# Optimization experiments

Hardware: AMD Instinct MI355X
Metric: run time of the kernel (lower is better)

## Reference

```python
import jax, jax.numpy as jnp
import numpy as np

H, D_NOPE, D_ROPE, D_V, L_KV, HID = 16, 128, 64, 128, 512, 2048
D_QK = D_NOPE + D_ROPE
THETA = 10000.0
EPS = 1e-6


def _rope(x, positions):
    # neox-style rotary over last dim (D_ROPE); x: [T, ..., D_ROPE]
    half = D_ROPE // 2
    inv_freq = 1.0 / (THETA ** (jnp.arange(half, dtype=jnp.float32) * 2.0 / D_ROPE))
    ang = positions.astype(jnp.float32)[:, None] * inv_freq[None, :]  # [T, half]
    shape = (x.shape[0],) + (1,) * (x.ndim - 2) + (half,)
    cos, sin = jnp.cos(ang).reshape(shape), jnp.sin(ang).reshape(shape)
    x1, x2 = x[..., :half], x[..., half:]
    return jnp.concatenate([x1 * cos - x2 * sin, x2 * cos + x1 * sin], axis=-1)


def _rmsnorm(x, w):
    var = jnp.mean(x * x, axis=-1, keepdims=True)
    return x * jax.lax.rsqrt(var + EPS) * w


def setup_inputs() -> dict:
    key = jax.random.key(0)
    ks = jax.random.split(key, 6)
    T = 4096
    s = lambda fan_in: 1.0 / np.sqrt(fan_in)
    return {
        "positions": jnp.arange(T, dtype=jnp.int32),
        "hidden_states": jax.random.normal(ks[0], (T, HID), jnp.float32),
        "Wq": jax.random.normal(ks[1], (HID, H * D_QK), jnp.float32) * s(HID),
        "Wkva": jax.random.normal(ks[2], (HID, L_KV + D_ROPE), jnp.float32) * s(HID),
        "kv_a_ln_w": jnp.ones((L_KV,), jnp.float32),
        "Wkvb": jax.random.normal(ks[3], (L_KV, H * (D_NOPE + D_V)), jnp.float32) * s(L_KV),
        "Wo": jax.random.normal(ks[4], (H * D_V, HID), jnp.float32) * s(H * D_V),
    }


def reference(positions, hidden_states, Wq, Wkva, kv_a_ln_w, Wkvb, Wo):
    T = hidden_states.shape[0]
    scaling = 1.0 / np.sqrt(D_QK)

    q = (hidden_states @ Wq).reshape(T, H, D_QK)
    q_nope, q_pe = q[..., :D_NOPE], q[..., D_NOPE:]

    latent = hidden_states @ Wkva                    # [T, L_KV + D_ROPE]
    kv_a = _rmsnorm(latent[:, :L_KV], kv_a_ln_w)     # [T, L_KV]
    k_pe = latent[:, L_KV:]                          # [T, D_ROPE] (shared across heads)

    kv = (kv_a @ Wkvb).reshape(T, H, D_NOPE + D_V)
    k_nope, v = kv[..., :D_NOPE], kv[..., D_NOPE:]

    q_pe = _rope(q_pe, positions)                    # [T, H, D_ROPE]
    k_pe = _rope(k_pe, positions)                    # [T, D_ROPE]

    q = jnp.concatenate([q_nope, q_pe], axis=-1)     # [T, H, D_QK]
    k = jnp.concatenate(
        [k_nope, jnp.broadcast_to(k_pe[:, None, :], (T, H, D_ROPE))], axis=-1)

    scores = jnp.einsum("thd,shd->hts", q, k) * scaling        # [H, T, T]
    causal = positions[:, None] >= positions[None, :]           # [T, T]
    scores = jnp.where(causal[None], scores, jnp.finfo(scores.dtype).min)
    attn = jax.nn.softmax(scores, axis=-1)
    out = jnp.einsum("hts,shd->thd", attn, v)                   # [T, H, D_V]
    return out.reshape(T, H * D_V) @ Wo                          # [T, HID]
```

## Files before the change

kernel.cpp:

```cpp
#include <hip/hip_runtime.h>
#include <hip/hip_bf16.h>

#define T_LEN 4096
#define HID_DIM 2048
#define NH 16
#define DNOPE 128
#define DROPE 64
#define DV 128
#define LKV 512
#define DQK 192

#define BN 64

typedef __attribute__((ext_vector_type(8))) __bf16 bf16x8;
typedef __attribute__((ext_vector_type(4))) float f32x4;
typedef __attribute__((ext_vector_type(4))) short s16x4;

__device__ __forceinline__ unsigned short f2b(float f) {
  unsigned u = __builtin_bit_cast(unsigned, f);
  unsigned r = (u + 0x7FFFu + ((u >> 16) & 1u)) >> 16;
  return (unsigned short)r;
}

#define GL2LDS16(gp, lp)                                                   \
  __builtin_amdgcn_global_load_lds(                                        \
      (const __attribute__((address_space(1))) unsigned int*)(gp),         \
      (__attribute__((address_space(3))) unsigned int*)(lp), 16, 0, 0)

#if __has_builtin(__builtin_amdgcn_mfma_f32_16x16x16bf16_1k)
#define HAVE_MFMA16 1
__device__ __forceinline__ f32x4 mfma16(s16x4 a, s16x4 b, f32x4 c) {
  return __builtin_amdgcn_mfma_f32_16x16x16bf16_1k(a, b, c, 0, 0, 0);
}
#elif __has_builtin(__builtin_amdgcn_mfma_f32_16x16x16_bf16)
#define HAVE_MFMA16 1
typedef __attribute__((ext_vector_type(4))) __bf16 bf16x4v;
__device__ __forceinline__ f32x4 mfma16(s16x4 a, s16x4 b, f32x4 c) {
  return __builtin_amdgcn_mfma_f32_16x16x16_bf16(
      __builtin_bit_cast(bf16x4v, a), __builtin_bit_cast(bf16x4v, b), c, 0, 0, 0);
}
#else
#define HAVE_MFMA16 0
#endif

__device__ __forceinline__ void xcd_swz(int nbx, int* bx, int* by) {
  int lin = blockIdx.y * nbx + blockIdx.x;
  int cpx = (nbx * gridDim.y) >> 3;
  int swz = (lin & 7) * cpx + (lin >> 3);
  *bx = swz % nbx;
  *by = swz / nbx;
}

__global__ void k_transpose_all(const float* __restrict__ Wq, const float* __restrict__ Wkva,
                                const float* __restrict__ Wkvb, const float* __restrict__ Wo,
                                const float* __restrict__ hs,
                                unsigned short* __restrict__ WqT, unsigned short* __restrict__ WkvaT,
                                unsigned short* __restrict__ WkvbT, unsigned short* __restrict__ WoT,
                                unsigned short* __restrict__ hsb) {
  int bid = blockIdx.x;
  int tx = threadIdx.x, ty = threadIdx.y;
  if (bid >= 13440) {
    int i = (bid - 13440) * 256 + ty * 32 + tx;
    const float4* in4 = (const float4*)hs;
    float4 v0 = in4[i * 2];
    float4 v1 = in4[i * 2 + 1];
    unsigned a = (unsigned)f2b(v0.x) | ((unsigned)f2b(v0.y) << 16);
    unsigned b = (unsigned)f2b(v0.z) | ((unsigned)f2b(v0.w) << 16);
    unsigned c = (unsigned)f2b(v1.x) | ((unsigned)f2b(v1.y) << 16);
    unsigned d = (unsigned)f2b(v1.z) | ((unsigned)f2b(v1.w) << 16);
    uint4 pk = {a, b, c, d};
    ((uint4*)hsb)[i] = pk;
    return;
  }
  __shared__ float t[32][33];
  const float* in; unsigned short* out; int R, C, bx, by;
  if (bid < 6144)      { in = Wq;   out = WqT;   R = 2048; C = 3072; bx = bid % 96;  by = bid / 96; }
  else if (bid < 7296) { int b = bid - 6144; in = Wkva; out = WkvaT; R = 2048; C = 576;  bx = b % 18;  by = b / 18; }
  else if (bid < 9344) { int b = bid - 7296; in = Wkvb; out = WkvbT; R = 512;  C = 4096; bx = b % 128; by = b / 128; }
  else                 { int b = bid - 9344; in = Wo;   out = WoT;   R = 2048; C = 2048; bx = b % 64;  by = b / 64; }
  int c0 = bx * 32, r0 = by * 32;
#pragma unroll
  for (int k = 0; k < 4; k++)
    t[ty + 8 * k][tx] = in[(size_t)(r0 + ty + 8 * k) * C + c0 + tx];
  __syncthreads();
  int u = ty * 32 + tx;
  int co = u >> 3;
  int rg = u & 7;
  unsigned lo = (unsigned)f2b(t[rg * 4 + 0][co]) | ((unsigned)f2b(t[rg * 4 + 1][co]) << 16);
  unsigned hi = (unsigned)f2b(t[rg * 4 + 2][co]) | ((unsigned)f2b(t[rg * 4 + 3][co]) << 16);
  uint2 pk = {lo, hi};
  *(uint2*)&out[(size_t)(c0 + co) * R + r0 + rg * 4] = pk;
}

#define GEMM_CORE(Aptr, Btptr, Nn, Kk, ldaa, ldbb)                                         \
  __shared__ unsigned short As[128 * 64];                                                  \
  __shared__ unsigned short Bs[128 * 64];                                                  \
  int tid = threadIdx.x;                                                                   \
  int lane = tid & 63, w = tid >> 6;                                                       \
  int quad = lane >> 4, l16 = lane & 15;                                                   \
  int wm = (w >> 1) * 64, wn = (w & 1) * 64;                                               \
  size_t aoff[4], boff[4];                                                                 \
  _Pragma("unroll")                                                                        \
  for (int k = 0; k < 4; k++) {                                                            \
    int c = tid + k * 256;                                                                 \
    int row = c >> 3, sc = c & 7;                                                          \
    int cg = sc ^ (row & 7);                                                               \
    aoff[k] = (size_t)(m0 + row) * (ldaa) + cg * 8;                                        \
    int bR = n0 + row; if (bR >= (Nn)) bR = (Nn) - 1;                                      \
    boff[k] = (size_t)bR * (ldbb) + cg * 8;                                                \
  }                                                                                        \
  f32x4 acc[4][4] = {};                                                                    \
  for (int k0 = 0; k0 < (Kk); k0 += 64) {                                                  \
    _Pragma("unroll")                                                                      \
    for (int k = 0; k < 4; k++) {                                                          \
      GL2LDS16((Aptr) + aoff[k] + k0, &As[(tid + k * 256) * 8]);                           \
      GL2LDS16((Btptr) + boff[k] + k0, &Bs[(tid + k * 256) * 8]);                          \
    }                                                                                      \
    __syncthreads();                                                                       \
    _Pragma("unroll")                                                                      \
    for (int ks = 0; ks < 2; ks++) {                                                       \
      bf16x8 aF[4], bF[4];                                                                 \
      _Pragma("unroll")                                                                    \
      for (int i = 0; i < 4; i++) {                                                        \
        int rowa = wm + i * 16 + l16;                                                      \
        aF[i] = *(const bf16x8*)&As[rowa * 64 + (((ks * 4 + quad) ^ (rowa & 7)) * 8)];     \
      }                                                                                    \
      _Pragma("unroll")                                                                    \
      for (int j = 0; j < 4; j++) {                                                        \
        int rowb = wn + j * 16 + l16;                                                      \
        bF[j] = *(const bf16x8*)&Bs[rowb * 64 + (((ks * 4 + quad) ^ (rowb & 7)) * 8)];     \
      }                                                                                    \
      _Pragma("unroll")                                                                    \
      for (int i = 0; i < 4; i++)                                                          \
        _Pragma("unroll")                                                                  \
        for (int j = 0; j < 4; j++)                                                        \
          acc[i][j] = __builtin_amdgcn_mfma_f32_16x16x32_bf16(aF[i], bF[j], acc[i][j], 0, 0, 0); \
    }                                                                                      \
    __syncthreads();                                                                       \
  }                                                                                        \
  int row0 = m0 + wm + quad * 4; (void)row0;

__global__ __launch_bounds__(256) void k_gemm128(
    const unsigned short* __restrict__ A, const unsigned short* __restrict__ Bt,
    float* __restrict__ Cf, int N, int K, int lda, int ldb, int ldc) {
  int bxs, bys; xcd_swz(gridDim.x, &bxs, &bys);
  int m0 = bys * 128, n0 = bxs * 128;
  GEMM_CORE(A, Bt, N, K, lda, ldb)
#pragma unroll
  for (int i = 0; i < 4; i++)
#pragma unroll
    for (int j = 0; j < 4; j++) {
      int col = n0 + wn + j * 16 + l16;
      if (col < N)
#pragma unroll
        for (int r = 0; r < 4; r++)
          Cf[(size_t)(row0 + i * 16 + r) * ldc + col] = acc[i][j][r];
    }
}

__global__ __launch_bounds__(256) void k_gemm_proj(
    const unsigned short* __restrict__ A, const unsigned short* __restrict__ WqT,
    const unsigned short* __restrict__ WkvaT, const int* __restrict__ pos,
    unsigned short* __restrict__ Qh, float* __restrict__ latentf) {
  int bxx, byy; xcd_swz(gridDim.x, &bxx, &byy);
  bool iswq = bxx < 24;
  const unsigned short* Bt = iswq ? WqT : WkvaT;
  int N = iswq ? NH * DQK : (LKV + DROPE);
  int m0 = byy * 128, n0 = (iswq ? bxx : bxx - 24) * 128;
  GEMM_CORE(A, Bt, N, HID_DIM, HID_DIM, HID_DIM)
  if (iswq) {
    const float scale = 0.07216878364870323f;
    int b64 = (n0 + wn) >> 6;
    int h = b64 / 3, rem3 = b64 - 3 * h;
    unsigned short* Qb = Qh + (size_t)h * T_LEN * DQK;
    if (rem3 < 2) {
#pragma unroll
      for (int i = 0; i < 4; i++)
#pragma unroll
        for (int r = 0; r < 4; r++) {
          int t = row0 + i * 16 + r;
#pragma unroll
          for (int j = 0; j < 4; j++)
            Qb[(size_t)t * DQK + rem3 * 64 + j * 16 + l16] = f2b(acc[i][j][r] * scale);
        }
    } else {
      float inv0 = __expf((float)l16 * -0.2878231366242557f);
      float inv1 = __expf((float)(16 + l16) * -0.2878231366242557f);
#pragma unroll
      for (int i = 0; i < 4; i++)
#pragma unroll
        for (int r = 0; r < 4; r++) {
          int t = row0 + i * 16 + r;
          float p = (float)pos[t];
#pragma unroll
          for (int j = 0; j < 2; j++) {
            int idx = j * 16 + l16;
            float inv = (j == 0) ? inv0 : inv1;
            float sn, cs;
            __sincosf(p * inv, &sn, &cs);
            float x1 = acc[i][j][r] * scale, x2 = acc[i][j + 2][r] * scale;
            Qb[(size_t)t * DQK + DNOPE + idx]      = f2b(x1 * cs - x2 * sn);
            Qb[(size_t)t * DQK + DNOPE + 32 + idx] = f2b(x2 * cs + x1 * sn);
          }
        }
    }
  } else {
#pragma unroll
    for (int i = 0; i < 4; i++)
#pragma unroll
      for (int j = 0; j < 4; j++) {
        int col = n0 + wn + j * 16 + l16;
        if (col < LKV + DROPE)
#pragma unroll
          for (int r = 0; r < 4; r++)
            latentf[(size_t)(row0 + i * 16 + r) * (LKV + DROPE) + col] = acc[i][j][r];
      }
  }
}

__global__ __launch_bounds__(256) void k_gemm_wkvb(
    const unsigned short* __restrict__ A, const unsigned short* __restrict__ Bt,
    unsigned short* __restrict__ Kh, unsigned short* __restrict__ VT) {
  int bxs, bys; xcd_swz(gridDim.x, &bxs, &bys);
  int m0 = bys * 128, n0 = bxs * 128;
  GEMM_CORE(A, Bt, NH * 256, LKV, LKV, LKV)
#pragma unroll
  for (int i = 0; i < 4; i++)
#pragma unroll
    for (int j = 0; j < 4; j++) {
      int col = n0 + wn + j * 16 + l16;
      int h = col >> 8, c = col & 255;
      int t0 = row0 + i * 16;
      if (c < 128) {
#pragma unroll
        for (int r = 0; r < 4; r++)
          Kh[((size_t)h * T_LEN + t0 + r) * DQK + c] = f2b(acc[i][j][r]);
      } else {
        unsigned lo = (unsigned)f2b(acc[i][j][0]) | ((unsigned)f2b(acc[i][j][1]) << 16);
        unsigned hi = (unsigned)f2b(acc[i][j][2]) | ((unsigned)f2b(acc[i][j][3]) << 16);
        uint2 pk = {lo, hi};
        *(uint2*)&VT[(size_t)(h * 128 + c - 128) * T_LEN + t0] = pk;
      }
    }
}

__global__ __launch_bounds__(256) void k_prep_latent(
    const float* __restrict__ latent, const float* __restrict__ w,
    const int* __restrict__ pos,
    unsigned short* __restrict__ kva, unsigned short* __restrict__ Kh) {
  int t = blockIdx.x * 4 + (threadIdx.x >> 6);
  int lane = threadIdx.x & 63;
  const float* row = latent + (size_t)t * (LKV + DROPE);
  f32x4 a = *(const f32x4*)&row[lane * 8];
  f32x4 b = *(const f32x4*)&row[lane * 8 + 4];
  float ss = a[0] * a[0] + a[1] * a[1] + a[2] * a[2] + a[3] * a[3] +
             b[0] * b[0] + b[1] * b[1] + b[2] * b[2] + b[3] * b[3];
  ss += __shfl_xor(ss, 1, 64);
  ss += __shfl_xor(ss, 2, 64);
  ss += __shfl_xor(ss, 4, 64);
  ss += __shfl_xor(ss, 8, 64);
  ss += __shfl_xor(ss, 16, 64);
  ss += __shfl_xor(ss, 32, 64);
  float rs = rsqrtf(ss / (float)LKV + 1e-6f);
  f32x4 w0 = *(const f32x4*)&w[lane * 8];
  f32x4 w1 = *(const f32x4*)&w[lane * 8 + 4];
  unsigned q0 = (unsigned)f2b(a[0] * rs * w0[0]) | ((unsigned)f2b(a[1] * rs * w0[1]) << 16);
  unsigned q1 = (unsigned)f2b(a[2] * rs * w0[2]) | ((unsigned)f2b(a[3] * rs * w0[3]) << 16);
  unsigned q2 = (unsigned)f2b(b[0] * rs * w1[0]) | ((unsigned)f2b(b[1] * rs * w1[1]) << 16);
  unsigned q3 = (unsigned)f2b(b[2] * rs * w1[2]) | ((unsigned)f2b(b[3] * rs * w1[3]) << 16);
  uint4 pk = {q0, q1, q2, q3};
  *(uint4*)&kva[(size_t)t * LKV + lane * 8] = pk;

  int i = lane;
  float p = (float)pos[t];
  float val;
  if (i < 32) {
    float x1 = row[LKV + i], x2 = row[LKV + i + 32];
    float inv = __expf(-(float)i * 0.2878231366242557f);
    float sn, cs; __sincosf(p * inv, &sn, &cs);
    val = x1 * cs - x2 * sn;
  } else {
    float x1 = row[LKV + i - 32], x2 = row[LKV + i];
    float inv = __expf(-(float)(i - 32) * 0.2878231366242557f);
    float sn, cs; __sincosf(p * inv, &sn, &cs);
    val = x2 * cs + x1 * sn;
  }
  unsigned short vb = f2b(val);
#pragma unroll
  for (int h = 0; h < NH; h++)
    Kh[((size_t)h * T_LEN + t) * DQK + DNOPE + i] = vb;
}

__global__ __launch_bounds__(256, 2) void k_flash(
    const unsigned short* __restrict__ Qh, const unsigned short* __restrict__ Kh,
    const unsigned short* __restrict__ VT, unsigned short* __restrict__ attn) {
  int bx = blockIdx.x;
  int h = bx & 15;
  int t = (bx & 255) >> 4;
  int qb = (bx < 256) ? (31 - t) : t;
  int m0 = qb * 128;
  int diagA = 2 * qb, diagB = 2 * qb + 1;
  int NT = 2 * qb + 2;

  __shared__ unsigned short Ks[2 * 64 * 24 * 8];
  __shared__ unsigned short Vs[2 * 128 * 8 * 8];

  int tid = threadIdx.x, lane = tid & 63, w = tid >> 6;
  int quad = lane >> 4, l16 = lane & 15;
  int x = l16 & 7;

  const unsigned short* Qbase = Qh + (size_t)h * T_LEN * DQK;
  const unsigned short* Kbase = Kh + (size_t)h * T_LEN * DQK;
  const unsigned short* Vbase = VT + (size_t)h * DV * T_LEN;

  bf16x8 qfS[6], qfL[6];
#pragma unroll
  for (int kk = 0; kk < 6; kk++) {
    qfS[kk] = *(const bf16x8*)(Qbase + (size_t)(m0 + w * 16 + l16) * DQK + kk * 32 + quad * 8);
    qfL[kk] = *(const bf16x8*)(Qbase + (size_t)(m0 + 64 + w * 16 + l16) * DQK + kk * 32 + quad * 8);
  }

  int koff[6], voff[4];
#pragma unroll
  for (int k = 0; k < 6; k++) {
    int c = tid + k * 256;
    int row = c / 24, sc = c - row * 24;
    int cg = (sc & 0x18) | ((sc ^ row) & 7);
    koff[k] = row * DQK + cg * 8;
  }
#pragma unroll
  for (int k = 0; k < 4; k++) {
    int c = tid + k * 256;
    int row = c >> 3, sc = c & 7;
    int cg = sc ^ (row & 7);
    voff[k] = row * T_LEN + cg * 8;
  }

  int kEo[4], kOo[4], vAo[4];
#pragma unroll
  for (int st = 0; st < 4; st++) {
    int rb = (st * 16 + l16) * 192;
    kEo[st] = rb + ((quad ^ x) * 8);
    kOo[st] = rb + (((quad + 4) ^ x) * 8);
    vAo[st] = l16 * 64 + (((st * 2 + (quad >> 1)) ^ x) * 8) + (quad & 1) * 4;
  }

  f32x4 OaccS[8] = {}, OaccL[8] = {};
  float liS = 0.f, liL = 0.f;
  int mS = m0 + w * 16 + l16;
  int mL = mS + 64;

#if !HAVE_MFMA16
  int lA = l16 + ((quad & 1) << 5);
  int lB = lA + 16;
  bool lowq = (quad < 2);
  int vFo[2];
#pragma unroll
  for (int u = 0; u < 2; u++)
    vFo[u] = l16 * 64 + (((u * 4 + quad) ^ x) * 8);
#endif

#define STAGE(buf)                                                                         \
  do {                                                                                     \
    unsigned short* ksd = Ks + (buf) * (64 * 24 * 8);                                      \
    unsigned short* vsd = Vs + (buf) * (128 * 8 * 8);                                      \
    _Pragma("unroll")                                                                      \
    for (int k = 0; k < 6; k++) GL2LDS16(Kbase + koff[k], &ksd[(tid + k * 256) * 8]);      \
    _Pragma("unroll")                                                                      \
    for (int k = 0; k < 4; k++) GL2LDS16(Vbase + voff[k], &vsd[(tid + k * 256) * 8]);      \
    _Pragma("unroll")                                                                      \
    for (int k = 0; k < 6; k++) koff[k] += BN * DQK;                                       \
    _Pragma("unroll")                                                                      \
    for (int k = 0; k < 4; k++) voff[k] += BN;                                             \
  } while (0)

#define PIPE_BARRIER()                                                                     \
  do {                                                                                     \
    asm volatile("s_waitcnt vmcnt(0)" ::: "memory");                                       \
    __builtin_amdgcn_s_barrier();                                                          \
    __builtin_amdgcn_sched_barrier(0);                                                     \
  } while (0)

  STAGE(0);
  PIPE_BARRIER();

  int cur = 0;
  for (int j = 0; j < NT; ++j) {
    if (j + 1 < NT) STAGE(cur ^ 1);

    const unsigned short* KsB = Ks + cur * (64 * 24 * 8);
    const unsigned short* VsB = Vs + cur * (128 * 8 * 8);

    f32x4 ScS[4] = {}, ScL[4] = {};
#pragma unroll
    for (int kk = 0; kk < 6; kk++) {
#pragma unroll
      for (int st = 0; st < 4; st++) {
        bf16x8 kb = *(const bf16x8*)(KsB + ((kk & 1) ? kOo[st] : kEo[st]) + (kk >> 1) * 64);
        ScS[st] = __builtin_amdgcn_mfma_f32_16x16x32_bf16(kb, qfS[kk], ScS[st], 0, 0, 0);
        ScL[st] = __builtin_amdgcn_mfma_f32_16x16x32_bf16(kb, qfL[kk], ScL[st], 0, 0, 0);
      }
    }

    int n0 = j * BN;
    if (j >= diagA) {
#pragma unroll
      for (int st = 0; st < 4; st++)
#pragma unroll
        for (int r = 0; r < 4; r++) {
          int s = n0 + st * 16 + quad * 4 + r;
          if (s > mS) ScS[st][r] = -1e30f;
        }
    }
    if (j == diagB) {
#pragma unroll
      for (int st = 0; st < 4; st++)
#pragma unroll
        for (int r = 0; r < 4; r++) {
          int s = n0 + st * 16 + quad * 4 + r;
          if (s > mL) ScL[st][r] = -1e30f;
        }
    }

    unsigned p0S[4], p1S[4], p0L[4], p1L[4];
#pragma unroll
    for (int st = 0; st < 4; st++) {
      float e0 = __expf(ScS[st][0]);
      float e1 = __expf(ScS[st][1]);
      float e2 = __expf(ScS[st][2]);
      float e3 = __expf(ScS[st][3]);
      liS += (e0 + e1) + (e2 + e3);
      p0S[st] = __builtin_amdgcn_perm(__builtin_bit_cast(unsigned, e1),
                                      __builtin_bit_cast(unsigned, e0), 0x07060302u);
      p1S[st] = __builtin_amdgcn_perm(__builtin_bit_cast(unsigned, e3),
                                      __builtin_bit_cast(unsigned, e2), 0x07060302u);
      float f0 = __expf(ScL[st][0]);
      float f1 = __expf(ScL[st][1]);
      float f2 = __expf(ScL[st][2]);
      float f3 = __expf(ScL[st][3]);
      liL += (f0 + f1) + (f2 + f3);
      p0L[st] = __builtin_amdgcn_perm(__builtin_bit_cast(unsigned, f1),
                                      __builtin_bit_cast(unsigned, f0), 0x07060302u);
      p1L[st] = __builtin_amdgcn_perm(__builtin_bit_cast(unsigned, f3),
                                      __builtin_bit_cast(unsigned, f2), 0x07060302u);
    }

#if HAVE_MFMA16
#pragma unroll
    for (int st = 0; st < 4; st++) {
      uint2 puS; puS.x = p0S[st]; puS.y = p1S[st];
      s16x4 pbS = __builtin_bit_cast(s16x4, puS);
      uint2 puL; puL.x = p0L[st]; puL.y = p1L[st];
      s16x4 pbL = __builtin_bit_cast(s16x4, puL);
#pragma unroll
      for (int dt = 0; dt < 8; dt++) {
        s16x4 va = __builtin_bit_cast(s16x4, *(const uint2*)(VsB + vAo[st] + dt * 1024));
        OaccS[dt] = mfma16(va, pbS, OaccS[dt]);
        OaccL[dt] = mfma16(va, pbL, OaccL[dt]);
      }
    }
#else
#pragma unroll
    for (int u = 0; u < 2; u++) {
      int a0 = __shfl((int)p0S[2 * u], lA, 64);
      int a1 = __shfl((int)p0S[2 * u + 1], lA, 64);
      int b0 = __shfl((int)p1S[2 * u], lA, 64);
      int b1 = __shfl((int)p1S[2 * u + 1], lA, 64);
      int c0 = __shfl((int)p0S[2 * u], lB, 64);
      int c1 = __shfl((int)p0S[2 * u + 1], lB, 64);
      int d0 = __shfl((int)p1S[2 * u], lB, 64);
      int d1 = __shfl((int)p1S[2 * u + 1], lB, 64);
      int4 pkS;
      pkS.x = lowq ? a0 : a1; pkS.y = lowq ? b0 : b1;
      pkS.z = lowq ? c0 : c1; pkS.w = lowq ? d0 : d1;
      bf16x8 pbS = __builtin_bit_cast(bf16x8, pkS);
      int sa0 = __shfl((int)p0L[2 * u], lA, 64);
      int sa1 = __shfl((int)p0L[2 * u + 1], lA, 64);
      int sb0 = __shfl((int)p1L[2 * u], lA, 64);
      int sb1 = __shfl((int)p1L[2 * u + 1], lA, 64);
      int sc0 = __shfl((int)p0L[2 * u], lB, 64);
      int sc1 = __shfl((int)p0L[2 * u + 1], lB, 64);
      int sd0 = __shfl((int)p1L[2 * u], lB, 64);
      int sd1 = __shfl((int)p1L[2 * u + 1], lB, 64);
      int4 pkL;
      pkL.x = lowq ? sa0 : sa1; pkL.y = lowq ? sb0 : sb1;
      pkL.z = lowq ? sc0 : sc1; pkL.w = lowq ? sd0 : sd1;
      bf16x8 pbL = __builtin_bit_cast(bf16x8, pkL);
#pragma unroll
      for (int dt = 0; dt < 8; dt++) {
        bf16x8 va = *(const bf16x8*)(VsB + vFo[u] + dt * 1024);
        OaccS[dt] = __builtin_amdgcn_mfma_f32_16x16x32_bf16(va, pbS, OaccS[dt], 0, 0, 0);
        OaccL[dt] = __builtin_amdgcn_mfma_f32_16x16x32_bf16(va, pbL, OaccL[dt], 0, 0, 0);
      }
    }
#endif

    PIPE_BARRIER();
    cur ^= 1;
  }

  liS += __shfl_xor(liS, 16, 64);
  liS += __shfl_xor(liS, 32, 64);
  liL += __shfl_xor(liL, 16, 64);
  liL += __shfl_xor(liL, 32, 64);

  float invS = 1.f / liS;
  float invL = 1.f / liL;
  unsigned short* dstS = attn + (size_t)mS * HID_DIM + h * DV + quad * 4;
  unsigned short* dstL = attn + (size_t)mL * HID_DIM + h * DV + quad * 4;
#pragma unroll
  for (int dt = 0; dt < 8; dt++) {
    unsigned lo = (unsigned)f2b(OaccS[dt][0] * invS) |
                  ((unsigned)f2b(OaccS[dt][1] * invS) << 16);
    unsigned hi = (unsigned)f2b(OaccS[dt][2] * invS) |
                  ((unsigned)f2b(OaccS[dt][3] * invS) << 16);
    uint2 pkv = {lo, hi};
    *(uint2*)(dstS + dt * 16) = pkv;
    unsigned lo2 = (unsigned)f2b(OaccL[dt][0] * invL) |
                   ((unsigned)f2b(OaccL[dt][1] * invL) << 16);
    unsigned hi2 = (unsigned)f2b(OaccL[dt][2] * invL) |
                   ((unsigned)f2b(OaccL[dt][3] * invL) << 16);
    uint2 pkv2 = {lo2, hi2};
    *(uint2*)(dstL + dt * 16) = pkv2;
  }
#undef STAGE
#undef PIPE_BARRIER
}

extern "C" void kernel_launch(void* const* d_in, const int* in_sizes, int n_in,
                              void* d_out, int out_size, void* d_ws, size_t ws_size,
                              hipStream_t stream) {
  const int*   positions = (const int*)d_in[0];
  const float* hs   = (const float*)d_in[1];
  const float* Wq   = (const float*)d_in[2];
  const float* Wkva = (const float*)d_in[3];
  const float* lnw  = (const float*)d_in[4];
  const float* Wkvb = (const float*)d_in[5];
  const float* Wo   = (const float*)d_in[6];
  float* out = (float*)d_out;

  char* p = (char*)d_ws;
  size_t off = 0;
  auto alloc = [&](size_t bytes) {
    char* r = p + off;
    off = (off + bytes + 255) & ~(size_t)255;
    return r;
  };
  unsigned short* hsb     = (unsigned short*)alloc((size_t)T_LEN * HID_DIM * 2);
  unsigned short* WqT     = (unsigned short*)alloc((size_t)(NH * DQK) * HID_DIM * 2);
  unsigned short* WkvaT   = (unsigned short*)alloc((size_t)(LKV + DROPE) * HID_DIM * 2);
  unsigned short* WkvbT   = (unsigned short*)alloc((size_t)(NH * 256) * LKV * 2);
  unsigned short* WoT     = (unsigned short*)alloc((size_t)HID_DIM * HID_DIM * 2);
  unsigned short* Qh      = (unsigned short*)alloc((size_t)NH * T_LEN * DQK * 2);
  unsigned short* kva     = (unsigned short*)alloc((size_t)T_LEN * LKV * 2);
  unsigned short* Kh      = (unsigned short*)alloc((size_t)NH * T_LEN * DQK * 2);
  unsigned short* VT      = (unsigned short*)alloc((size_t)NH * DV * T_LEN * 2);
  unsigned short* attn    = (unsigned short*)alloc((size_t)T_LEN * HID_DIM * 2);
  float*          latentf = (float*)alloc((size_t)T_LEN * (LKV + DROPE) * 4);

  k_transpose_all<<<17536, dim3(32, 8), 0, stream>>>(Wq, Wkva, Wkvb, Wo, hs,
                                                     WqT, WkvaT, WkvbT, WoT, hsb);

  k_gemm_proj<<<dim3(29, T_LEN / 128), 256, 0, stream>>>(hsb, WqT, WkvaT, positions, Qh, latentf);

  k_prep_latent<<<T_LEN / 4, 256, 0, stream>>>(latentf, lnw, positions, kva, Kh);

  k_gemm_wkvb<<<dim3((NH * 256) / 128, T_LEN / 128), 256, 0, stream>>>(kva, WkvbT, Kh, VT);

  k_flash<<<dim3(512), 256, 0, stream>>>(Qh, Kh, VT, attn);

  k_gemm128<<<dim3(HID_DIM / 128, T_LEN / 128), 256, 0, stream>>>(
      attn, WoT, out, HID_DIM, HID_DIM, HID_DIM, HID_DIM, HID_DIM);
}
```

Baseline: 428.4 us.

## Double-buffer LDS in GEMM core to overlap global loads with MFMA

The shared GEMM macro now keeps two LDS stages for A and B. It issues the next k-tile's global-to-LDS loads before computing on the current tile, and replaces the two syncthreads per iteration with a single vmcnt wait plus barrier. This aims to hide global load latency behind the MFMA work in the projection, Wkvb and output GEMMs. The cost is twice the LDS footprint, 64KB per block, and the launch bounds now request 2 blocks per CU, which may limit occupancy or registers.

```diff
diff --git a/kernel.cpp b/kernel.cpp
--- a/kernel.cpp
+++ b/kernel.cpp
@@ -92,13 +92,31 @@
   *(uint2*)&out[(size_t)(c0 + co) * R + r0 + rg * 4] = pk;
 }
 
+#define GBAR()                                                                             \
+  do {                                                                                     \
+    asm volatile("s_waitcnt vmcnt(0)" ::: "memory");                                       \
+    __builtin_amdgcn_s_barrier();                                                          \
+    __builtin_amdgcn_sched_barrier(0);                                                     \
+  } while (0)
+
+#define GEMM_STAGE(buf, kk0)                                                               \
+  do {                                                                                     \
+    _Pragma("unroll")                                                                      \
+    for (int k = 0; k < 4; k++) {                                                          \
+      GL2LDS16(APTR_ + aoff[k] + (kk0), &As[(buf) * 8192 + (tid + k * 256) * 8]);          \
+      GL2LDS16(BPTR_ + boff[k] + (kk0), &Bs[(buf) * 8192 + (tid + k * 256) * 8]);          \
+    }                                                                                      \
+  } while (0)
+
 #define GEMM_CORE(Aptr, Btptr, Nn, Kk, ldaa, ldbb)                                         \
-  __shared__ unsigned short As[128 * 64];                                                  \
-  __shared__ unsigned short Bs[128 * 64];                                                  \
+  __shared__ unsigned short As[2 * 128 * 64];                                              \
+  __shared__ unsigned short Bs[2 * 128 * 64];                                              \
   int tid = threadIdx.x;                                                                   \
   int lane = tid & 63, w = tid >> 6;                                                       \
   int quad = lane >> 4, l16 = lane & 15;                                                   \
   int wm = (w >> 1) * 64, wn = (w & 1) * 64;                                               \
+  const unsigned short* APTR_ = (Aptr);                                                    \
+  const unsigned short* BPTR_ = (Btptr);                                                   \
   size_t aoff[4], boff[4];                                                                 \
   _Pragma("unroll")                                                                        \
   for (int k = 0; k < 4; k++) {                                                            \
@@ -110,25 +128,25 @@
     boff[k] = (size_t)bR * (ldbb) + cg * 8;                                                \
   }                                                                                        \
   f32x4 acc[4][4] = {};                                                                    \
+  GEMM_STAGE(0, 0);                                                                        \
+  GBAR();                                                                                  \
+  int cur = 0;                                                                             \
   for (int k0 = 0; k0 < (Kk); k0 += 64) {                                                  \
-    _Pragma("unroll")                                                                      \
-    for (int k = 0; k < 4; k++) {                                                          \
-      GL2LDS16((Aptr) + aoff[k] + k0, &As[(tid + k * 256) * 8]);                           \
-      GL2LDS16((Btptr) + boff[k] + k0, &Bs[(tid + k * 256) * 8]);                          \
-    }                                                                                      \
-    __syncthreads();                                                                       \
+    if (k0 + 64 < (Kk)) GEMM_STAGE(cur ^ 1, k0 + 64);                                      \
+    const unsigned short* AsB = As + cur * 8192;                                           \
+    const unsigned short* BsB = Bs + cur * 8192;                                           \
     _Pragma("unroll")                                                                      \
     for (int ks = 0; ks < 2; ks++) {                                                       \
       bf16x8 aF[4], bF[4];                                                                 \
       _Pragma("unroll")                                                                    \
       for (int i = 0; i < 4; i++) {                                                        \
         int rowa = wm + i * 16 + l16;                                                      \
-        aF[i] = *(const bf16x8*)&As[rowa * 64 + (((ks * 4 + quad) ^ (rowa & 7)) * 8)];     \
+        aF[i] = *(const bf16x8*)&AsB[rowa * 64 + (((ks * 4 + quad) ^ (rowa & 7)) * 8)];    \
       }                                                                                    \
       _Pragma("unroll")                                                                    \
       for (int j = 0; j < 4; j++) {                                                        \
         int rowb = wn + j * 16 + l16;                                                      \
-        bF[j] = *(const bf16x8*)&Bs[rowb * 64 + (((ks * 4 + quad) ^ (rowb & 7)) * 8)];     \
+        bF[j] = *(const bf16x8*)&BsB[rowb * 64 + (((ks * 4 + quad) ^ (rowb & 7)) * 8)];    \
       }                                                                                    \
       _Pragma("unroll")                                                                    \
       for (int i = 0; i < 4; i++)                                                          \
@@ -136,11 +154,12 @@
         for (int j = 0; j < 4; j++)                                                        \
           acc[i][j] = __builtin_amdgcn_mfma_f32_16x16x32_bf16(aF[i], bF[j], acc[i][j], 0, 0, 0); \
     }                                                                                      \
-    __syncthreads();                                                                       \
+    GBAR();                                                                                \
+    cur ^= 1;                                                                              \
   }                                                                                        \
   int row0 = m0 + wm + quad * 4; (void)row0;
 
-__global__ __launch_bounds__(256) void k_gemm128(
+__global__ __launch_bounds__(256, 2) void k_gemm128(
     const unsigned short* __restrict__ A, const unsigned short* __restrict__ Bt,
     float* __restrict__ Cf, int N, int K, int lda, int ldb, int ldc) {
   int bxs, bys; xcd_swz(gridDim.x, &bxs, &bys);
@@ -158,7 +177,7 @@
     }
 }
 
-__global__ __launch_bounds__(256) void k_gemm_proj(
+__global__ __launch_bounds__(256, 2) void k_gemm_proj(
     const unsigned short* __restrict__ A, const unsigned short* __restrict__ WqT,
     const unsigned short* __restrict__ WkvaT, const int* __restrict__ pos,
     unsigned short* __restrict__ Qh, float* __restrict__ latentf) {
@@ -218,7 +237,7 @@
   }
 }
 
-__global__ __launch_bounds__(256) void k_gemm_wkvb(
+__global__ __launch_bounds__(256, 2) void k_gemm_wkvb(
     const unsigned short* __restrict__ A, const unsigned short* __restrict__ Bt,
     unsigned short* __restrict__ Kh, unsigned short* __restrict__ VT) {
   int bxs, bys; xcd_swz(gridDim.x, &bxs, &bys);
```

Measured after the change: 415.2 us. 3.1% less time.
